# Optimization experiments

Measured on AMD Instinct MI355X. Metric: run time of the kernel, lower is better.

The kernel has to match this reference:

```python
import jax, jax.numpy as jnp
import numpy as np
import math

H = 768
NH = 12
D = H // NH


def setup_inputs() -> dict:
    key = jax.random.key(0)
    ks = jax.random.split(key, 13)
    B, S = 1, 384
    s = 0.02
    inp = {
        "hidden_states": jax.random.normal(ks[0], (B, S, H), jnp.float32),
        "attention_mask": jnp.zeros((B, 1, 1, S), jnp.float32),
        "pos_emb": jax.random.normal(ks[1], (B, S, S, H), jnp.float32),
        "Wq": jax.random.normal(ks[2], (H, H), jnp.float32) * s,
        "bq": jnp.zeros((H,), jnp.float32),
        "Wk": jax.random.normal(ks[3], (H, H), jnp.float32) * s,
        "bk": jnp.zeros((H,), jnp.float32),
        "Wv": jax.random.normal(ks[4], (H, H), jnp.float32) * s,
        "bv": jnp.zeros((H,), jnp.float32),
        "Wpk": jax.random.normal(ks[5], (H, H), jnp.float32) * s,
        "bpk": jnp.zeros((H,), jnp.float32),
        "Wpq": jax.random.normal(ks[6], (H, H), jnp.float32) * s,
        "bpq": jnp.zeros((H,), jnp.float32),
    }
    return inp


def reference(hidden_states, attention_mask, pos_emb,
              Wq, bq, Wk, bk, Wv, bv, Wpk, bpk, Wpq, bpq):
    B, S, Hd = hidden_states.shape
    split = lambda x: x.reshape(B, S, NH, D).transpose(0, 2, 1, 3)  # -> (B, h, S, d)
    q = split(hidden_states @ Wq + bq)
    k = split(hidden_states @ Wk + bk)
    v = split(hidden_states @ Wv + bv)

    # content-to-content
    c2c = jnp.einsum('bhid,bhjd->bhij', q, k)

    # per-pair position projections: (B,S,S,H) -> (B,S,S,h,d)
    pos_key = (pos_emb @ Wpk + bpk).reshape(B, S, S, NH, D)
    pos_query = (pos_emb @ Wpq + bpq).reshape(B, S, S, NH, D)

    # content-to-position: q[b,h,i,:] . pos_key[b,i,j,h,:]
    c2p = jnp.einsum('bhid,bijhd->bhij', q, pos_key)
    # position-to-content: pos_query[b,j,i,h,:] . k[b,h,j,:]
    p2c = jnp.einsum('bjihd,bhjd->bhij', pos_query, k)

    scores = (c2c + c2p + p2c) / math.sqrt(D) + attention_mask
    probs = jax.nn.softmax(scores, axis=-1)  # dropout is identity (p=0 / eval)
    ctx = jnp.einsum('bhij,bhjd->bhid', probs, v)
    return ctx.transpose(0, 2, 1, 3).reshape(B, S, Hd)
```

## Files before the change

kernel.cpp:

```cpp
#include <hip/hip_runtime.h>
#include <math.h>

#define SEQ 384
#define HDIM 768
#define NHEAD 12
#define DHEAD 64

__global__ __launch_bounds__(256)
void qkv_gemm(const float* __restrict__ X,
              const float* __restrict__ Wq, const float* __restrict__ bq,
              const float* __restrict__ Wk, const float* __restrict__ bk,
              const float* __restrict__ Wv, const float* __restrict__ bv,
              float* __restrict__ q, float* __restrict__ k, float* __restrict__ v)
{
    __shared__ float Xs[128 * 68];
    const int z = blockIdx.z;
    const float* W    = (z == 0) ? Wq : (z == 1) ? Wk : Wv;
    const float* bias = (z == 0) ? bq : (z == 1) ? bk : bv;
    float* out        = (z == 0) ? q  : (z == 1) ? k  : v;

    const int m0 = blockIdx.x * 64;
    const int n0 = blockIdx.y * 64;
    const int tid = threadIdx.x;
    const int ty = tid / 16, tx = tid % 16;

    const int lm = tid >> 2;
    const int lc = (tid & 3) * 4;

    float acc[4][4] = {};

    for (int k0 = 0; k0 < HDIM; k0 += 128) {
        float4 xa[8];
        #pragma unroll
        for (int it = 0; it < 8; it++)
            xa[it] = *(const float4*)&X[(size_t)(m0 + lm) * HDIM + k0 + it * 16 + lc];
        __syncthreads();
        #pragma unroll
        for (int it = 0; it < 8; it++) {
            const int kk = it * 16 + lc;
            Xs[(kk + 0) * 68 + lm] = xa[it].x;
            Xs[(kk + 1) * 68 + lm] = xa[it].y;
            Xs[(kk + 2) * 68 + lm] = xa[it].z;
            Xs[(kk + 3) * 68 + lm] = xa[it].w;
        }
        __syncthreads();
        const float* Wp = &W[(size_t)k0 * HDIM + n0 + 4 * tx];
        #pragma unroll 8
        for (int kk = 0; kk < 128; kk++) {
            float4 b4 = *(const float4*)&Wp[(size_t)kk * HDIM];
            float4 a4 = *(const float4*)&Xs[kk * 68 + 4 * ty];
            float a[4] = {a4.x, a4.y, a4.z, a4.w};
            float b[4] = {b4.x, b4.y, b4.z, b4.w};
            #pragma unroll
            for (int ia = 0; ia < 4; ia++)
                #pragma unroll
                for (int ib = 0; ib < 4; ib++)
                    acc[ia][ib] = fmaf(a[ia], b[ib], acc[ia][ib]);
        }
    }
    float4 bv4 = *(const float4*)&bias[n0 + 4 * tx];
    #pragma unroll
    for (int ia = 0; ia < 4; ia++) {
        float4 o;
        o.x = acc[ia][0] + bv4.x; o.y = acc[ia][1] + bv4.y;
        o.z = acc[ia][2] + bv4.z; o.w = acc[ia][3] + bv4.w;
        *(float4*)&out[(size_t)(m0 + 4 * ty + ia) * HDIM + n0 + 4 * tx] = o;
    }
}

__global__ __launch_bounds__(256)
void proj_all(const float* __restrict__ q, const float* __restrict__ k,
              const float* __restrict__ Wpk, const float* __restrict__ Wpq,
              const float* __restrict__ bpq, const float* __restrict__ bpk,
              const float* __restrict__ mask,
              float* __restrict__ qp, float* __restrict__ kp,
              float* __restrict__ CC)
{
    __shared__ float As[64][68];
    __shared__ float Bs[64][68];
    __shared__ float cterm_s;
    const int z = blockIdx.z;
    const int tid = threadIdx.x;
    const int dg = tid % 16, row = tid / 16;
    const int ty = tid / 16, tx = tid % 16;

    if (z < 24) {
        const int h = z % NHEAD;
        const int s = z / NHEAD;
        const float* Asrc = s ? k   : q;
        const float* Wsrc = s ? Wpq : Wpk;
        float* out        = s ? kp  : qp;
        const int i0 = blockIdx.x * 64, e0 = blockIdx.y * 64;

        #pragma unroll
        for (int r = 0; r < 4; r++) {
            const int rr = r * 16 + row;
            float4 a4 = *(const float4*)&Asrc[(size_t)(i0 + rr) * HDIM + h * 64 + dg * 4];
            float4 b4 = *(const float4*)&Wsrc[(size_t)(e0 + rr) * HDIM + h * 64 + dg * 4];
            As[dg * 4 + 0][rr] = a4.x; As[dg * 4 + 1][rr] = a4.y;
            As[dg * 4 + 2][rr] = a4.z; As[dg * 4 + 3][rr] = a4.w;
            Bs[dg * 4 + 0][rr] = b4.x; Bs[dg * 4 + 1][rr] = b4.y;
            Bs[dg * 4 + 2][rr] = b4.z; Bs[dg * 4 + 3][rr] = b4.w;
        }
        __syncthreads();

        float acc[4][4] = {};
        #pragma unroll 4
        for (int d = 0; d < 64; d++) {
            float4 a4 = *(const float4*)&As[d][4 * ty];
            float4 b4 = *(const float4*)&Bs[d][4 * tx];
            float a[4] = {a4.x, a4.y, a4.z, a4.w};
            float b[4] = {b4.x, b4.y, b4.z, b4.w};
            #pragma unroll
            for (int ia = 0; ia < 4; ia++)
                #pragma unroll
                for (int ib = 0; ib < 4; ib++)
                    acc[ia][ib] = fmaf(a[ia], b[ib], acc[ia][ib]);
        }
        #pragma unroll
        for (int ia = 0; ia < 4; ia++) {
            float4 o = make_float4(acc[ia][0], acc[ia][1], acc[ia][2], acc[ia][3]);
            *(float4*)&out[((size_t)(i0 + 4 * ty + ia) * NHEAD + h) * HDIM + e0 + 4 * tx] = o;
        }
    } else {
        if (blockIdx.y >= 6) return;
        const int h  = z - 24;
        const int i0 = blockIdx.x * 64, j0 = blockIdx.y * 64;

        const float4 bq4 = *(const float4*)&bpq[h * 64 + dg * 4];
        const float4 bk4 = *(const float4*)&bpk[h * 64 + dg * 4];
        #pragma unroll
        for (int r = 0; r < 4; r++) {
            const int rr = r * 16 + row;
            float4 q4 = *(const float4*)&q[(size_t)(i0 + rr) * HDIM + h * 64 + dg * 4];
            float4 k4 = *(const float4*)&k[(size_t)(j0 + rr) * HDIM + h * 64 + dg * 4];
            As[dg * 4 + 0][rr] = q4.x + bq4.x; As[dg * 4 + 1][rr] = q4.y + bq4.y;
            As[dg * 4 + 2][rr] = q4.z + bq4.z; As[dg * 4 + 3][rr] = q4.w + bq4.w;
            Bs[dg * 4 + 0][rr] = k4.x + bk4.x; Bs[dg * 4 + 1][rr] = k4.y + bk4.y;
            Bs[dg * 4 + 2][rr] = k4.z + bk4.z; Bs[dg * 4 + 3][rr] = k4.w + bk4.w;
        }
        if (tid < 64) {
            float pc = bpq[h * 64 + tid] * bpk[h * 64 + tid];
            #pragma unroll
            for (int o = 32; o; o >>= 1) pc += __shfl_xor(pc, o);
            if (tid == 0) cterm_s = pc;
        }
        __syncthreads();

        float acc[4][4] = {};
        #pragma unroll 4
        for (int d = 0; d < 64; d++) {
            float4 a4 = *(const float4*)&As[d][4 * ty];
            float4 b4 = *(const float4*)&Bs[d][4 * tx];
            float a[4] = {a4.x, a4.y, a4.z, a4.w};
            float b[4] = {b4.x, b4.y, b4.z, b4.w};
            #pragma unroll
            for (int ia = 0; ia < 4; ia++)
                #pragma unroll
                for (int ib = 0; ib < 4; ib++)
                    acc[ia][ib] = fmaf(a[ia], b[ib], acc[ia][ib]);
        }
        const float cterm = cterm_s;
        const float4 m4 = *(const float4*)&mask[j0 + 4 * tx];
        #pragma unroll
        for (int ia = 0; ia < 4; ia++) {
            float4 o;
            o.x = (acc[ia][0] - cterm) * 0.125f + m4.x;
            o.y = (acc[ia][1] - cterm) * 0.125f + m4.y;
            o.z = (acc[ia][2] - cterm) * 0.125f + m4.z;
            o.w = (acc[ia][3] - cterm) * 0.125f + m4.w;
            *(float4*)&CC[((size_t)h * SEQ + i0 + 4 * ty + ia) * SEQ + j0 + 4 * tx] = o;
        }
    }
}

__global__ __launch_bounds__(256, 3)
void scores_pos(const float* __restrict__ pe, const float* __restrict__ qp,
                const float* __restrict__ kp,
                float* __restrict__ A1, float* __restrict__ P2T)
{
    __shared__ float lds[32 * 200];
    const int i    = blockIdx.x;
    const int jh   = blockIdx.y;
    const int tid  = threadIdx.x;
    const int lane = tid & 63;
    const int wave = tid >> 6;
    const int rgu = __builtin_amdgcn_readfirstlane(wave >> 1);
    const int esu = __builtin_amdgcn_readfirstlane(wave & 1);

    const float* pebase = pe + ((size_t)i * SEQ + jh * 192) * HDIM;
    const float* wb = (rgu ? kp : qp) + (size_t)i * NHEAD * HDIM;

    const int wr  = tid >> 3;
    const int wec = tid & 7;

    float acc[12][3] = {};
    float4 ga[6], gb[6];

    auto loadc = [&](float4* g, int c) {
        const int e0 = c * 32;
        #pragma unroll
        for (int rnd = 0; rnd < 3; rnd++) {
            const int jb = rnd * 64 + wr * 2;
            g[2 * rnd + 0] = *(const float4*)&pebase[(size_t)jb * HDIM + e0 + wec * 4];
            g[2 * rnd + 1] = *(const float4*)&pebase[(size_t)(jb + 1) * HDIM + e0 + wec * 4];
        }
    };
    auto writec = [&](const float4* g) {
        #pragma unroll
        for (int rnd = 0; rnd < 3; rnd++) {
            const int jb = rnd * 64 + wr * 2;
            const float4 g0 = g[2 * rnd], g1 = g[2 * rnd + 1];
            *(float2*)&lds[(wec * 4 + 0) * 200 + jb] = make_float2(g0.x, g1.x);
            *(float2*)&lds[(wec * 4 + 1) * 200 + jb] = make_float2(g0.y, g1.y);
            *(float2*)&lds[(wec * 4 + 2) * 200 + jb] = make_float2(g0.z, g1.z);
            *(float2*)&lds[(wec * 4 + 3) * 200 + jb] = make_float2(g0.w, g1.w);
        }
    };
    auto compute = [&](int c) {
        const float* wc = wb + c * 32 + esu * 16;
        #pragma unroll 4
        for (int ee = 0; ee < 16; ee++) {
            const int ei = esu * 16 + ee;
            float2 p2 = *(const float2*)&lds[ei * 200 + 2 * lane];
            float  p1 = lds[ei * 200 + 128 + lane];
            #pragma unroll
            for (int r = 0; r < 12; r++) {
                const float w = wc[r * HDIM + ee];
                acc[r][0] = fmaf(w, p2.x, acc[r][0]);
                acc[r][1] = fmaf(w, p2.y, acc[r][1]);
                acc[r][2] = fmaf(w, p1,   acc[r][2]);
            }
        }
    };

    loadc(ga, 0);
    #pragma unroll 1
    for (int cc = 0; cc < 12; cc++) {
        loadc(gb, 2 * cc + 1);
        __syncthreads();
        writec(ga);
        __syncthreads();
        if (cc < 11) loadc(ga, 2 * cc + 2);
        compute(2 * cc);
        __syncthreads();
        writec(gb);
        __syncthreads();
        compute(2 * cc + 1);
    }

    __syncthreads();
    if (esu == 1) {
        #pragma unroll
        for (int r = 0; r < 12; r++) {
            const int row = rgu * 12 + r;
            *(float2*)&lds[row * 200 + 2 * lane] = make_float2(acc[r][0], acc[r][1]);
            lds[row * 200 + 128 + lane] = acc[r][2];
        }
    }
    __syncthreads();
    if (esu == 0) {
        #pragma unroll
        for (int r = 0; r < 12; r++) {
            const int row = rgu * 12 + r;
            float2 o2 = *(const float2*)&lds[row * 200 + 2 * lane];
            float  o1 = lds[row * 200 + 128 + lane];
            o2.x += acc[r][0]; o2.y += acc[r][1]; o1 += acc[r][2];
            *(float2*)&lds[row * 200 + 2 * lane] = o2;
            lds[row * 200 + 128 + lane] = o1;
        }
    }
    __syncthreads();

    for (int t = tid; t < 24 * 48; t += 256) {
        const int row = t / 48;
        const int c4  = (t % 48) * 4;
        float4 o = *(const float4*)&lds[row * 200 + c4];
        o.x *= 0.125f; o.y *= 0.125f; o.z *= 0.125f; o.w *= 0.125f;
        float* dst = (row < 12)
            ? &A1[((size_t)row * SEQ + i) * SEQ + jh * 192 + c4]
            : &P2T[((size_t)(row - 12) * SEQ + i) * SEQ + jh * 192 + c4];
        *(float4*)dst = o;
    }
}

__global__ __launch_bounds__(256)
void fold_transpose(const float* __restrict__ CC, const float* __restrict__ A1,
                    const float* __restrict__ P2T, float* __restrict__ S)
{
    __shared__ float T[64 * 65];
    const int h  = blockIdx.z;
    const int i0 = blockIdx.x * 64, j0 = blockIdx.y * 64;
    const int tid = threadIdx.x;
    const int c = tid % 16, r = tid / 16;

    #pragma unroll
    for (int p = 0; p < 4; p++) {
        const int jr = p * 16 + r;
        float4 t4 = *(const float4*)&P2T[((size_t)h * SEQ + j0 + jr) * SEQ + i0 + 4 * c];
        T[(4 * c + 0) * 65 + jr] = t4.x;
        T[(4 * c + 1) * 65 + jr] = t4.y;
        T[(4 * c + 2) * 65 + jr] = t4.z;
        T[(4 * c + 3) * 65 + jr] = t4.w;
    }
    __syncthreads();
    #pragma unroll
    for (int p = 0; p < 4; p++) {
        const int ir = p * 16 + r;
        const size_t off = ((size_t)h * SEQ + i0 + ir) * SEQ + j0 + 4 * c;
        float4 cc4 = *(const float4*)&CC[off];
        float4 a4  = *(const float4*)&A1[off];
        float4 o;
        o.x = cc4.x + a4.x + T[ir * 65 + 4 * c + 0];
        o.y = cc4.y + a4.y + T[ir * 65 + 4 * c + 1];
        o.z = cc4.z + a4.z + T[ir * 65 + 4 * c + 2];
        o.w = cc4.w + a4.w + T[ir * 65 + 4 * c + 3];
        *(float4*)&S[off] = o;
    }
}

__global__ __launch_bounds__(384)
void attn_out(const float* __restrict__ S, const float* __restrict__ v,
              float* __restrict__ out)
{
    const int i = blockIdx.x, h = blockIdx.y;
    const int tid = threadIdx.x;
    __shared__ float p_s[SEQ];
    __shared__ float redm[6], reds[6];
    __shared__ float redvf[24 * 64];

    float sc = S[((size_t)h * SEQ + i) * SEQ + tid];

    const int lane = tid & 63, w = tid >> 6;
    float m = sc;
    #pragma unroll
    for (int o = 32; o; o >>= 1) m = fmaxf(m, __shfl_xor(m, o));
    if (lane == 0) redm[w] = m;
    __syncthreads();
    m = redm[0];
    #pragma unroll
    for (int t = 1; t < 6; t++) m = fmaxf(m, redm[t]);

    float p = __expf(sc - m);
    float sum = p;
    #pragma unroll
    for (int o = 32; o; o >>= 1) sum += __shfl_xor(sum, o);
    if (lane == 0) reds[w] = sum;
    p_s[tid] = p;
    __syncthreads();
    const float SUM = reds[0] + reds[1] + reds[2] + reds[3] + reds[4] + reds[5];

    const int dq = lane & 15, jsub = lane >> 4;
    const int j0 = w * 64;
    float4 av = make_float4(0.f, 0.f, 0.f, 0.f);
    #pragma unroll 8
    for (int jj = 0; jj < 16; jj++) {
        const int j = j0 + jj * 4 + jsub;
        float4 v4 = *(const float4*)&v[(size_t)j * HDIM + h * 64 + dq * 4];
        const float pj = p_s[j];
        av.x = fmaf(pj, v4.x, av.x); av.y = fmaf(pj, v4.y, av.y);
        av.z = fmaf(pj, v4.z, av.z); av.w = fmaf(pj, v4.w, av.w);
    }
    *(float4*)&redvf[(w * 4 + jsub) * 64 + dq * 4] = av;
    __syncthreads();
    if (tid < 64) {
        float o = 0.f;
        #pragma unroll
        for (int r = 0; r < 24; r++) o += redvf[r * 64 + tid];
        out[(size_t)i * HDIM + h * 64 + tid] = o / SUM;
    }
}

extern "C" void kernel_launch(void* const* d_in, const int* in_sizes, int n_in,
                              void* d_out, int out_size, void* d_ws, size_t ws_size,
                              hipStream_t stream)
{
    const float* hs   = (const float*)d_in[0];
    const float* mask = (const float*)d_in[1];
    const float* pe   = (const float*)d_in[2];
    const float* Wq   = (const float*)d_in[3];
    const float* bq   = (const float*)d_in[4];
    const float* Wk   = (const float*)d_in[5];
    const float* bk   = (const float*)d_in[6];
    const float* Wv   = (const float*)d_in[7];
    const float* bv   = (const float*)d_in[8];
    const float* Wpk  = (const float*)d_in[9];
    const float* bpk  = (const float*)d_in[10];
    const float* Wpq  = (const float*)d_in[11];
    const float* bpq  = (const float*)d_in[12];

    float* ws = (float*)d_ws;
    const size_t SZ_QKV = (size_t)SEQ * HDIM;
    const size_t SZ_QP  = (size_t)SEQ * NHEAD * HDIM;
    const size_t SZ_SC  = (size_t)NHEAD * SEQ * SEQ;
    float* q   = ws;
    float* k   = q  + SZ_QKV;
    float* v   = k  + SZ_QKV;
    float* qp  = v  + SZ_QKV;
    float* kp  = qp + SZ_QP;
    float* A1  = kp + SZ_QP;
    float* P2T = A1 + SZ_SC;
    float* CC  = P2T + SZ_SC;
    float* S   = CC + SZ_SC;

    qkv_gemm<<<dim3(6, 12, 3), 256, 0, stream>>>(hs, Wq, bq, Wk, bk, Wv, bv, q, k, v);
    proj_all<<<dim3(6, 12, 36), 256, 0, stream>>>(q, k, Wpk, Wpq, bpq, bpk, mask,
                                                  qp, kp, CC);
    scores_pos<<<dim3(SEQ, 2), 256, 0, stream>>>(pe, qp, kp, A1, P2T);
    fold_transpose<<<dim3(6, 6, 12), 256, 0, stream>>>(CC, A1, P2T, S);
    attn_out<<<dim3(SEQ, NHEAD), 384, 0, stream>>>(S, v, (float*)d_out);
}
```

Before: 790.4 us.

## Fuse score fold into softmax kernel and reorder projected-weight layout

Removes the fold_transpose kernel and the S buffer: attn_out now sums CC, A1 and the transposed P2T directly. Each block handles four query rows, so every V load is reused across them. The projection GEMM also writes qp/kp in a permuted layout, so scores_pos reads weights with a small contiguous stride instead of an HDIM stride. The P2T read in attn_out is a strided column gather, which may be less coalesced than the old tiled transpose.

```diff
diff --git a/kernel.cpp b/kernel.cpp
--- a/kernel.cpp
+++ b/kernel.cpp
@@ -5,6 +5,7 @@
 #define HDIM 768
 #define NHEAD 12
 #define DHEAD 64
+#define GI 4
 
 __global__ __launch_bounds__(256)
 void qkv_gemm(const float* __restrict__ X,
@@ -117,10 +118,12 @@
                 for (int ib = 0; ib < 4; ib++)
                     acc[ia][ib] = fmaf(a[ia], b[ib], acc[ia][ib]);
         }
+        const int e = e0 + 4 * tx;
+        const int off = (e >> 5) * 384 + ((e >> 4) & 1) * 192 + h * 16 + (e & 15);
         #pragma unroll
         for (int ia = 0; ia < 4; ia++) {
             float4 o = make_float4(acc[ia][0], acc[ia][1], acc[ia][2], acc[ia][3]);
-            *(float4*)&out[((size_t)(i0 + 4 * ty + ia) * NHEAD + h) * HDIM + e0 + 4 * tx] = o;
+            *(float4*)&out[(size_t)(i0 + 4 * ty + ia) * (NHEAD * HDIM) + off] = o;
         }
     } else {
         if (blockIdx.y >= 6) return;
@@ -218,7 +221,7 @@
         }
     };
     auto compute = [&](int c) {
-        const float* wc = wb + c * 32 + esu * 16;
+        const float* wc = wb + c * 384 + esu * 192;
         #pragma unroll 4
         for (int ee = 0; ee < 16; ee++) {
             const int ei = esu * 16 + ee;
@@ -226,7 +229,7 @@
             float  p1 = lds[ei * 200 + 128 + lane];
             #pragma unroll
             for (int r = 0; r < 12; r++) {
-                const float w = wc[r * HDIM + ee];
+                const float w = wc[r * 16 + ee];
                 acc[r][0] = fmaf(w, p2.x, acc[r][0]);
                 acc[r][1] = fmaf(w, p2.y, acc[r][1]);
                 acc[r][2] = fmaf(w, p1,   acc[r][2]);
@@ -284,90 +287,81 @@
     }
 }
 
-__global__ __launch_bounds__(256)
-void fold_transpose(const float* __restrict__ CC, const float* __restrict__ A1,
-                    const float* __restrict__ P2T, float* __restrict__ S)
-{
-    __shared__ float T[64 * 65];
-    const int h  = blockIdx.z;
-    const int i0 = blockIdx.x * 64, j0 = blockIdx.y * 64;
-    const int tid = threadIdx.x;
-    const int c = tid % 16, r = tid / 16;
-
-    #pragma unroll
-    for (int p = 0; p < 4; p++) {
-        const int jr = p * 16 + r;
-        float4 t4 = *(const float4*)&P2T[((size_t)h * SEQ + j0 + jr) * SEQ + i0 + 4 * c];
-        T[(4 * c + 0) * 65 + jr] = t4.x;
-        T[(4 * c + 1) * 65 + jr] = t4.y;
-        T[(4 * c + 2) * 65 + jr] = t4.z;
-        T[(4 * c + 3) * 65 + jr] = t4.w;
-    }
-    __syncthreads();
-    #pragma unroll
-    for (int p = 0; p < 4; p++) {
-        const int ir = p * 16 + r;
-        const size_t off = ((size_t)h * SEQ + i0 + ir) * SEQ + j0 + 4 * c;
-        float4 cc4 = *(const float4*)&CC[off];
-        float4 a4  = *(const float4*)&A1[off];
-        float4 o;
-        o.x = cc4.x + a4.x + T[ir * 65 + 4 * c + 0];
-        o.y = cc4.y + a4.y + T[ir * 65 + 4 * c + 1];
-        o.z = cc4.z + a4.z + T[ir * 65 + 4 * c + 2];
-        o.w = cc4.w + a4.w + T[ir * 65 + 4 * c + 3];
-        *(float4*)&S[off] = o;
-    }
-}
-
 __global__ __launch_bounds__(384)
-void attn_out(const float* __restrict__ S, const float* __restrict__ v,
+void attn_out(const float* __restrict__ CC, const float* __restrict__ A1,
+              const float* __restrict__ P2T, const float* __restrict__ v,
               float* __restrict__ out)
 {
-    const int i = blockIdx.x, h = blockIdx.y;
+    const int i0 = blockIdx.x * GI, h = blockIdx.y;
     const int tid = threadIdx.x;
-    __shared__ float p_s[SEQ];
-    __shared__ float redm[6], reds[6];
-    __shared__ float redvf[24 * 64];
-
-    float sc = S[((size_t)h * SEQ + i) * SEQ + tid];
+    __shared__ float p_s[GI][SEQ];
+    __shared__ float redm[GI][6], reds[GI][6];
+    __shared__ float redvf[GI][24 * 64];
 
     const int lane = tid & 63, w = tid >> 6;
-    float m = sc;
-    #pragma unroll
-    for (int o = 32; o; o >>= 1) m = fmaxf(m, __shfl_xor(m, o));
-    if (lane == 0) redm[w] = m;
-    __syncthreads();
-    m = redm[0];
-    #pragma unroll
-    for (int t = 1; t < 6; t++) m = fmaxf(m, redm[t]);
-
-    float p = __expf(sc - m);
-    float sum = p;
-    #pragma unroll
-    for (int o = 32; o; o >>= 1) sum += __shfl_xor(sum, o);
-    if (lane == 0) reds[w] = sum;
-    p_s[tid] = p;
-    __syncthreads();
-    const float SUM = reds[0] + reds[1] + reds[2] + reds[3] + reds[4] + reds[5];
+
+    float4 t4 = *(const float4*)&P2T[((size_t)h * SEQ + tid) * SEQ + i0];
+    float tt[GI] = {t4.x, t4.y, t4.z, t4.w};
+    float sc[GI];
+    #pragma unroll
+    for (int g = 0; g < GI; g++) {
+        const size_t off = ((size_t)h * SEQ + i0 + g) * SEQ + tid;
+        sc[g] = CC[off] + A1[off] + tt[g];
+    }
+
+    #pragma unroll
+    for (int g = 0; g < GI; g++) {
+        float m = sc[g];
+        #pragma unroll
+        for (int o = 32; o; o >>= 1) m = fmaxf(m, __shfl_xor(m, o));
+        if (lane == 0) redm[g][w] = m;
+    }
+    __syncthreads();
+    float SUMv[GI];
+    #pragma unroll
+    for (int g = 0; g < GI; g++) {
+        float m = redm[g][0];
+        #pragma unroll
+        for (int t = 1; t < 6; t++) m = fmaxf(m, redm[g][t]);
+        float p = __expf(sc[g] - m);
+        float sum = p;
+        #pragma unroll
+        for (int o = 32; o; o >>= 1) sum += __shfl_xor(sum, o);
+        if (lane == 0) reds[g][w] = sum;
+        p_s[g][tid] = p;
+    }
+    __syncthreads();
+    #pragma unroll
+    for (int g = 0; g < GI; g++)
+        SUMv[g] = reds[g][0] + reds[g][1] + reds[g][2] +
+                  reds[g][3] + reds[g][4] + reds[g][5];
 
     const int dq = lane & 15, jsub = lane >> 4;
     const int j0 = w * 64;
-    float4 av = make_float4(0.f, 0.f, 0.f, 0.f);
-    #pragma unroll 8
+    float4 av[GI] = {};
+    #pragma unroll 4
     for (int jj = 0; jj < 16; jj++) {
         const int j = j0 + jj * 4 + jsub;
         float4 v4 = *(const float4*)&v[(size_t)j * HDIM + h * 64 + dq * 4];
-        const float pj = p_s[j];
-        av.x = fmaf(pj, v4.x, av.x); av.y = fmaf(pj, v4.y, av.y);
-        av.z = fmaf(pj, v4.z, av.z); av.w = fmaf(pj, v4.w, av.w);
-    }
-    *(float4*)&redvf[(w * 4 + jsub) * 64 + dq * 4] = av;
+        #pragma unroll
+        for (int g = 0; g < GI; g++) {
+            const float pj = p_s[g][j];
+            av[g].x = fmaf(pj, v4.x, av[g].x); av[g].y = fmaf(pj, v4.y, av[g].y);
+            av[g].z = fmaf(pj, v4.z, av[g].z); av[g].w = fmaf(pj, v4.w, av[g].w);
+        }
+    }
+    #pragma unroll
+    for (int g = 0; g < GI; g++)
+        *(float4*)&redvf[g][(w * 4 + jsub) * 64 + dq * 4] = av[g];
     __syncthreads();
     if (tid < 64) {
-        float o = 0.f;
-        #pragma unroll
-        for (int r = 0; r < 24; r++) o += redvf[r * 64 + tid];
-        out[(size_t)i * HDIM + h * 64 + tid] = o / SUM;
+        #pragma unroll
+        for (int g = 0; g < GI; g++) {
+            float o = 0.f;
+            #pragma unroll
+            for (int r = 0; r < 24; r++) o += redvf[g][r * 64 + tid];
+            out[(size_t)(i0 + g) * HDIM + h * 64 + tid] = o / SUMv[g];
+        }
     }
 }
 
@@ -401,12 +395,10 @@
     float* A1  = kp + SZ_QP;
     float* P2T = A1 + SZ_SC;
     float* CC  = P2T + SZ_SC;
-    float* S   = CC + SZ_SC;
 
     qkv_gemm<<<dim3(6, 12, 3), 256, 0, stream>>>(hs, Wq, bq, Wk, bk, Wv, bv, q, k, v);
     proj_all<<<dim3(6, 12, 36), 256, 0, stream>>>(q, k, Wpk, Wpq, bpq, bpk, mask,
                                                   qp, kp, CC);
     scores_pos<<<dim3(SEQ, 2), 256, 0, stream>>>(pe, qp, kp, A1, P2T);
-    fold_transpose<<<dim3(6, 6, 12), 256, 0, stream>>>(CC, A1, P2T, S);
-    attn_out<<<dim3(SEQ, NHEAD), 384, 0, stream>>>(S, v, (float*)d_out);
+    attn_out<<<dim3(SEQ / GI, NHEAD), 384, 0, stream>>>(CC, A1, P2T, v, (float*)d_out);
 }
```

Measured after the change: 783.7 us (median of 2 runs). No clear change (-0.9%).
